# Kernel tuning notes

Hardware: AMD Instinct MI355X
Metric: run time of the kernel (lower is better)

The kernel has to match this reference:

```python
import jax, jax.numpy as jnp
import numpy as np

N, C, R = 100000, 128, 3
NUM_EMB = 3  # ceil((r+1)/2)+1 for r=3
E0, EL = 300000, 80000
SC = 0.05


def setup_inputs() -> dict:
    key = jax.random.key(0)
    ks = jax.random.split(key, 40)
    d = {}
    d["x"] = jax.random.normal(ks[0], (N, C), jnp.float32)
    # loopyN0: row 0 = sorted target node ids (CSR requirement), row 1 = neighbor ids
    t0 = jnp.sort(jax.random.randint(ks[1], (E0,), 0, N))
    s0 = jax.random.randint(ks[2], (E0,), 0, N)
    d["loopyN0"] = jnp.stack([t0, s0]).astype(jnp.int32)
    for L in range(1, R + 1):
        tgt = jnp.sort(jax.random.randint(ks[2 + 2 * L], (EL,), 0, N))
        rest = jax.random.randint(ks[3 + 2 * L], (L + 1, EL), 0, N)
        d[f"loopyN{L}"] = jnp.concatenate([tgt[None], rest]).astype(jnp.int32)
        d[f"loopyA{L}"] = jax.random.randint(ks[10 + L], (L + 2, EL), 0, NUM_EMB).astype(jnp.int32)
    # per-conv params (r=3 unshared CustomGINConv layers), stacked on leading axis
    d["emb"] = jax.random.normal(ks[20], (R, NUM_EMB, C)) * SC
    d["Wt"] = jax.random.normal(ks[21], (R, 2 * C, C)) * SC
    d["bt"] = jax.random.normal(ks[22], (R, C)) * SC
    d["mlp_w0"] = jax.random.normal(ks[23], (R, C, C)) * SC
    d["mlp_b0"] = jax.random.normal(ks[24], (R, C)) * SC
    d["mlp_w1"] = jax.random.normal(ks[25], (R, C, C)) * SC
    d["mlp_b1"] = jax.random.normal(ks[26], (R, C)) * SC
    d["conv_eps"] = jnp.ones((R,), jnp.float32)   # CustomGINConv eps init = ones(1)
    d["r_eps"] = jnp.zeros((R + 1,), jnp.float32)
    d["eps"] = jnp.zeros((), jnp.float32)
    # conv_final: MLP(C, C, num_layers=2, norm=Identity, relu)
    d["fin_w0"] = jax.random.normal(ks[27], (C, C)) * SC
    d["fin_b0"] = jax.random.normal(ks[28], (C,)) * SC
    d["fin_w1"] = jax.random.normal(ks[29], (C, C)) * SC
    d["fin_b1"] = jax.random.normal(ks[30], (C,)) * SC
    return d


def _mlp2(h, w0, b0, w1, b1):
    # MLP with num_layers=2, norm=Identity, relu
    h = h @ w0 + b0
    h = jax.nn.relu(h)
    return h @ w1 + b1


def reference(x, loopyN0, loopyN1, loopyN2, loopyN3, loopyA1, loopyA2, loopyA3,
              emb, Wt, bt, mlp_w0, mlp_b0, mlp_w1, mlp_b1,
              conv_eps, r_eps, eps, fin_w0, fin_b0, fin_w1, fin_b1):
    loopyN = [loopyN0, loopyN1, loopyN2, loopyN3]
    loopyA = [None, loopyA1, loopyA2, loopyA3]
    n_nodes = x.shape[0]
    # L = 0: plain neighbor sum (segment_csr over sorted targets == segment_sum)
    seg = jax.ops.segment_sum(x[loopyN0[1]], loopyN0[0], num_segments=n_nodes)
    rc = (1.0 + r_eps[0]) * seg
    for L in range(1, R + 1):
        nl = loopyN[L]
        cc = x[nl[1:]]                                  # [L+1, E, C] path-node gather
        at = loopyA[L][1:]                              # [L+1, E] atomic types
        i = L - 1
        h = jnp.concatenate([cc, emb[i][at]], axis=-1) @ Wt[i] + bt[i]   # [L+1, E, C]
        # custom_propagate: kernel [1,0,1] along path axis, zero 'same' padding
        hp = jnp.pad(h, ((1, 1), (0, 0), (0, 0)))
        y = hp[:-2] + hp[2:]
        o = _mlp2((1.0 + conv_eps[i]) * cc + y, mlp_w0[i], mlp_b0[i], mlp_w1[i], mlp_b1[i])
        o = o.sum(0)                                    # sum over path positions -> [E, C]
        seg = jax.ops.segment_sum(o, nl[0], num_segments=n_nodes)
        rc = rc + (1.0 + r_eps[L]) * seg
    return _mlp2((1.0 + eps) * x + rc, fin_w0, fin_b0, fin_w1, fin_b1)
```

## Files before the change

### kernel.cpp

```cpp
#include <hip/hip_runtime.h>
#include <stdint.h>

#define CDIM 128
#define NNODES 100000
#define E0EDGES 300000
#define ELEDGES 80000

typedef unsigned short u16;
typedef unsigned int u32;
typedef short bf16x8 __attribute__((ext_vector_type(8)));
typedef float f32x4 __attribute__((ext_vector_type(4)));

__device__ __forceinline__ float bf2f(u32 u){
  union { u32 i; float f; } v; v.i = u << 16; return v.f;
}
__device__ __forceinline__ float bf2f_hi(u32 u){
  union { u32 i; float f; } v; v.i = u & 0xffff0000u; return v.f;
}
__device__ __forceinline__ u16 f2bf(float f){
  u32 u = __builtin_bit_cast(u32, f);
  u32 r = (u + 0x7fffu + ((u >> 16) & 1u)) >> 16;
  return (u16)r;
}
__device__ __forceinline__ u32 pack2(float lo, float hi){
  return ((u32)f2bf(hi) << 16) | (u32)f2bf(lo);
}
__device__ __forceinline__ u32 cvtpk(float lo, float hi){
  u32 r;
  asm("v_cvt_pk_bf16_f32 %0, %1, %2" : "=v"(r) : "v"(lo), "v"(hi));
  return r;
}
template<int CTRL>
__device__ __forceinline__ float dppf(float v){
  int r = __builtin_amdgcn_update_dpp(0, __builtin_bit_cast(int, v), CTRL, 0xF, 0xF, true);
  return __builtin_bit_cast(float, r);
}
#define DPP_SHR1 0x111
#define DPP_SHL1 0x101
#define DPP_XOR1 0xB1
#define DPP_XOR2 0x4E

__device__ __forceinline__ int swzi(int r, int c){
  return r*CDIM + ((((c>>3) ^ (r&7)))<<3) + (c&7);
}
__device__ __forceinline__ int swz8(int r, int col0){
  int chunk = col0 >> 3;
  return r*CDIM + ((chunk ^ (r & 7)) << 3) + (col0 & 7);
}

__device__ __forceinline__ void gemm64(const u16* A, const u16* B, f32x4* acc, int wave, int lane){
  const int lr = lane & 15, g = lane >> 4;
  const int arow = wave*16 + lr;
#pragma unroll
  for (int ks = 0; ks < 4; ++ks){
    const int ach = ks*4 + g;
    bf16x8 a = *(const bf16x8*)&A[arow*CDIM + ((ach ^ (arow & 7)) << 3)];
#pragma unroll
    for (int ct = 0; ct < 8; ++ct){
      const int brow = ct*16 + lr;
      bf16x8 b = *(const bf16x8*)&B[brow*CDIM + ((ach ^ (brow & 7)) << 3)];
      acc[ct] = __builtin_amdgcn_mfma_f32_16x16x32_bf16(a, b, acc[ct], 0, 0, 0);
    }
  }
}

__device__ __forceinline__ void gemmS(const u16* W, const u16* Z, f32x4* acc, int zrow, int lane){
  const int lr = lane & 15, g = lane >> 4;
#pragma unroll
  for (int ks = 0; ks < 4; ++ks){
    const int ch = ks*4 + g;
    bf16x8 zb = *(const bf16x8*)&Z[zrow*CDIM + ((ch ^ (zrow & 7)) << 3)];
#pragma unroll
    for (int ct = 0; ct < 8; ++ct){
      const int wrow = ct*16 + lr;
      bf16x8 wb = *(const bf16x8*)&W[wrow*CDIM + ((ch ^ (wrow & 7)) << 3)];
      acc[ct] = __builtin_amdgcn_mfma_f32_16x16x32_bf16(wb, zb, acc[ct], 0, 0, 0);
    }
  }
}

__device__ __forceinline__ void stage_w(const u16* __restrict__ gsrc, u16* sdst, int tid){
  for (int c = tid; c < CDIM*16; c += 256){
    int r = c >> 4, ch = c & 15;
    *(uint4*)&sdst[(r*16 + (ch ^ (r & 7)))*8] = ((const uint4*)(gsrc + r*CDIM))[ch];
  }
}

__global__ __launch_bounds__(256) void xb_kernel(const float* __restrict__ x, u16* __restrict__ xb){
  int i = blockIdx.x*256 + threadIdx.x;
  size_t idx = (size_t)i*4;
  if (idx < (size_t)NNODES*CDIM){
    float4 v = *(const float4*)(x + idx);
    uint2 o; o.x = cvtpk(v.x, v.y); o.y = cvtpk(v.z, v.w);
    *(uint2*)(xb + idx) = o;
  }
}

__global__ __launch_bounds__(256) void prep_kernel(
    const float* __restrict__ Wt, const float* __restrict__ w0, const float* __restrict__ w1,
    const float* __restrict__ fw0, const float* __restrict__ fw1,
    const float* __restrict__ emb, const float* __restrict__ bt,
    u16* __restrict__ WtT, u16* __restrict__ w0T, u16* __restrict__ w1T,
    u16* __restrict__ fw0T, u16* __restrict__ fw1T, float* __restrict__ eWt)
{
  int tid = blockIdx.x*blockDim.x + threadIdx.x;
  int nt = gridDim.x*blockDim.x;
  for (int idx = tid; idx < 3*CDIM*CDIM; idx += nt){
    int i = idx/(CDIM*CDIM), rem = idx%(CDIM*CDIM), col = rem/CDIM, k = rem%CDIM;
    WtT[idx] = f2bf(Wt[(size_t)i*2*CDIM*CDIM + k*CDIM + col]);
    w0T[idx] = f2bf(w0[(size_t)i*CDIM*CDIM + k*CDIM + col]);
    w1T[idx] = f2bf(w1[(size_t)i*CDIM*CDIM + k*CDIM + col]);
  }
  for (int idx = tid; idx < CDIM*CDIM; idx += nt){
    int col = idx/CDIM, k = idx%CDIM;
    fw0T[idx] = f2bf(fw0[k*CDIM + col]);
    fw1T[idx] = f2bf(fw1[k*CDIM + col]);
  }
  for (int idx = tid; idx < 3*3*CDIM; idx += nt){
    int i = idx/(3*CDIM), a = (idx/CDIM)%3, c2 = idx%CDIM;
    float s = bt[i*CDIM + c2];
    for (int k = 0; k < CDIM; ++k)
      s += emb[(i*3 + a)*CDIM + k] * Wt[(size_t)i*2*CDIM*CDIM + (CDIM + k)*CDIM + c2];
    eWt[idx] = s;
  }
}

__global__ __launch_bounds__(256) void build_csr_kernel(
    const int* __restrict__ tgt, int ne, int* __restrict__ rowptr)
{
  int e = blockIdx.x*blockDim.x + threadIdx.x;
  if (e >= ne) return;
  int tc = tgt[e];
  int tp = (e == 0) ? -1 : tgt[e-1];
  for (int n = tp + 1; n <= tc; ++n) rowptr[n] = e;
  if (e == ne - 1){
    for (int n = tc + 1; n <= NNODES; ++n) rowptr[n] = ne;
  }
}

template<int L>
__global__ __launch_bounds__(512, 4) void layer_kernel(
    const u16* __restrict__ xb,
    const int* __restrict__ nl,
    const int* __restrict__ ai,
    const u16* __restrict__ WtT, const u16* __restrict__ w0T, const u16* __restrict__ w1T,
    const float* __restrict__ eWt,
    const float* __restrict__ b0g, const float* __restrict__ b1g,
    const float* __restrict__ cepsg,
    u16* __restrict__ oL)
{
  constexpr int RPE = (L == 1) ? 2 : 4;
  constexpr int TE  = 128 / RPE;
  constexpr int LI  = L - 1;
  __shared__ __align__(16) u16 sW[CDIM*CDIM];
  __shared__ __align__(16) u16 sA[128*CDIM];
  __shared__ __align__(16) float sE[3*136];
  __shared__ __align__(16) float b0s[CDIM];
  __shared__ __align__(16) float b1s[CDIM];

  const int tid  = threadIdx.x;
  const int wave = tid >> 6, lane = tid & 63;
  const int lr   = lane & 15, g = lane >> 4;
  const int row  = wave*16 + lr;
  const int e0   = blockIdx.x * TE;
  const int ed   = e0 + row / RPE;
  const int pos  = row % RPE;

  int node = -1, aid = 0;
  if (pos <= L){
    node = nl[(1 + pos)*ELEDGES + ed];
    aid  = ai[(1 + pos)*ELEDGES + ed];
  }
  const float mu = (pos > 0) ? 1.f : 0.f;
  const float md = (pos < L) ? 1.f : 0.f;
  const float ce = 1.0f + cepsg[LI];

  for (int c = tid; c < CDIM*16; c += 512){
    int r = c >> 4, ch = c & 15;
    *(uint4*)&sW[(r*16 + (ch ^ (r & 7)))*8] = ((const uint4*)(WtT + LI*CDIM*CDIM + r*CDIM))[ch];
  }
  for (int c = tid; c < 3*CDIM; c += 512) sE[(c>>7)*136 + (c&127)] = eWt[LI*3*CDIM + c];
  if (tid < CDIM) b0s[tid] = b0g[LI*CDIM + tid];
  else if (tid < 2*CDIM) b1s[tid-CDIM] = b1g[LI*CDIM + (tid-CDIM)];

  {
    const uint4* src = (const uint4*)(xb + (size_t)(node < 0 ? 0 : node)*CDIM);
#pragma unroll
    for (int i2 = 0; i2 < 4; ++i2){
      int ch = g*4 + i2;
      uint4 v = make_uint4(0u,0u,0u,0u);
      if (node >= 0) v = src[ch];
      *(uint4*)&sA[(row*16 + (ch ^ (row & 7)))*8] = v;
    }
  }
  __syncthreads();

  f32x4 acc[8];
#pragma unroll
  for (int ct = 0; ct < 8; ++ct) acc[ct] = (f32x4){0.f,0.f,0.f,0.f};
  gemmS(sW, sA, acc, row, lane);

  {
    const float* eWrow = &sE[aid*136];
#pragma unroll
    for (int ct = 0; ct < 8; ++ct){
      const int col0 = ct*16 + g*4;
      float4 ew = *(const float4*)&eWrow[col0];
      float h0 = acc[ct][0] + ew.x;
      float h1 = acc[ct][1] + ew.y;
      float h2 = acc[ct][2] + ew.z;
      float h3 = acc[ct][3] + ew.w;
      float u0 = dppf<DPP_SHR1>(h0), u1 = dppf<DPP_SHR1>(h1),
            u2 = dppf<DPP_SHR1>(h2), u3 = dppf<DPP_SHR1>(h3);
      float d0 = dppf<DPP_SHL1>(h0), d1 = dppf<DPP_SHL1>(h1),
            d2 = dppf<DPP_SHL1>(h2), d3 = dppf<DPP_SHL1>(h3);
      uint2 ccv = *(const uint2*)&sA[swz8(row, col0)];
      float c0 = bf2f(ccv.x & 0xffffu), c1 = bf2f_hi(ccv.x);
      float c2 = bf2f(ccv.y & 0xffffu), c3 = bf2f_hi(ccv.y);
      float z0 = ce*c0 + mu*u0 + md*d0;
      float z1 = ce*c1 + mu*u1 + md*d1;
      float z2 = ce*c2 + mu*u2 + md*d2;
      float z3 = ce*c3 + mu*u3 + md*d3;
      uint2 zv; zv.x = cvtpk(z0, z1); zv.y = cvtpk(z2, z3);
      *(uint2*)&sA[swz8(row, col0)] = zv;
    }
  }
  __syncthreads();
  for (int c = tid; c < CDIM*16; c += 512){
    int r = c >> 4, ch = c & 15;
    *(uint4*)&sW[(r*16 + (ch ^ (r & 7)))*8] = ((const uint4*)(w0T + LI*CDIM*CDIM + r*CDIM))[ch];
  }
  __syncthreads();

#pragma unroll
  for (int ct = 0; ct < 8; ++ct) acc[ct] = (f32x4){0.f,0.f,0.f,0.f};
  gemmS(sW, sA, acc, row, lane);

#pragma unroll
  for (int ct = 0; ct < 8; ++ct){
    const int col0 = ct*16 + g*4;
    float4 bb = *(const float4*)&b0s[col0];
    float t0 = acc[ct][0] + bb.x; t0 = t0 > 0.f ? t0 : 0.f;
    float t1 = acc[ct][1] + bb.y; t1 = t1 > 0.f ? t1 : 0.f;
    float t2 = acc[ct][2] + bb.z; t2 = t2 > 0.f ? t2 : 0.f;
    float t3 = acc[ct][3] + bb.w; t3 = t3 > 0.f ? t3 : 0.f;
    uint2 tv; tv.x = cvtpk(t0, t1); tv.y = cvtpk(t2, t3);
    *(uint2*)&sA[swz8(row, col0)] = tv;
  }
  __syncthreads();
  for (int c = tid; c < CDIM*16; c += 512){
    int r = c >> 4, ch = c & 15;
    *(uint4*)&sW[(r*16 + (ch ^ (r & 7)))*8] = ((const uint4*)(w1T + LI*CDIM*CDIM + r*CDIM))[ch];
  }
  __syncthreads();

#pragma unroll
  for (int ct = 0; ct < 8; ++ct) acc[ct] = (f32x4){0.f,0.f,0.f,0.f};
  gemmS(sW, sA, acc, row, lane);

  const float mz = (L == 2 && pos == 3) ? 0.f : 1.f;
#pragma unroll
  for (int ct = 0; ct < 8; ++ct){
    const int col0 = ct*16 + g*4;
    float v0 = mz*acc[ct][0], v1 = mz*acc[ct][1], v2 = mz*acc[ct][2], v3 = mz*acc[ct][3];
    v0 += dppf<DPP_XOR1>(v0); v1 += dppf<DPP_XOR1>(v1);
    v2 += dppf<DPP_XOR1>(v2); v3 += dppf<DPP_XOR1>(v3);
    if constexpr (RPE == 4){
      v0 += dppf<DPP_XOR2>(v0); v1 += dppf<DPP_XOR2>(v1);
      v2 += dppf<DPP_XOR2>(v2); v3 += dppf<DPP_XOR2>(v3);
    }
    if (pos == 0){
      float4 bb = *(const float4*)&b1s[col0];
      const float nb = (float)(L + 1);
      uint2 ov;
      ov.x = cvtpk(v0 + nb*bb.x, v1 + nb*bb.y);
      ov.y = cvtpk(v2 + nb*bb.z, v3 + nb*bb.w);
      *(uint2*)(oL + (size_t)ed*CDIM + col0) = ov;
    }
  }
}

__global__ __launch_bounds__(256) void gather_rc_kernel(
    const float* __restrict__ x,
    const int* __restrict__ s0,
    const int* __restrict__ rp0, const int* __restrict__ rp1,
    const int* __restrict__ rp2, const int* __restrict__ rp3,
    const u16* __restrict__ o1, const u16* __restrict__ o2, const u16* __restrict__ o3,
    const float* __restrict__ repsg, u16* __restrict__ rcb)
{
  const int wave = threadIdx.x >> 6, lane = threadIdx.x & 63;
  const int node = blockIdx.x*4 + wave;
  if (node >= NNODES) return;
  float a0 = 0.f, a1 = 0.f;
  {
    const float sc = 1.f + repsg[0];
    int lo = rp0[node], hi = rp0[node+1];
    for (int e = lo; e < hi; ++e){
      int s = s0[e];
      float2 v = *(const float2*)(x + (size_t)s*CDIM + lane*2);
      a0 += sc*v.x; a1 += sc*v.y;
    }
  }
  const u16* os[3]  = {o1, o2, o3};
  const int* rps[3] = {rp1, rp2, rp3};
#pragma unroll
  for (int li = 0; li < 3; ++li){
    const float sc = 1.f + repsg[1+li];
    int lo = rps[li][node], hi = rps[li][node+1];
    for (int e = lo; e < hi; ++e){
      u32 v = *(const u32*)(os[li] + (size_t)e*CDIM + lane*2);
      a0 += sc*bf2f(v & 0xffffu); a1 += sc*bf2f(v >> 16);
    }
  }
  *(u32*)(rcb + (size_t)node*CDIM + lane*2) = pack2(a0, a1);
}

__global__ __launch_bounds__(256) void final_kernel(
    const float* __restrict__ x, const u16* __restrict__ rc,
    const u16* __restrict__ fw0T, const u16* __restrict__ fw1T,
    const float* __restrict__ fb0, const float* __restrict__ fb1,
    const float* __restrict__ epsg, float* __restrict__ outp)
{
  __shared__ __align__(16) u16 sW[CDIM*CDIM];
  __shared__ __align__(16) u16 sA[64*CDIM];
  const int tid  = threadIdx.x;
  const int wave = tid >> 6, lane = tid & 63;
  const int lr   = lane & 15, g = lane >> 4;
  const int r0   = blockIdx.x * 64;
  const float se = 1.0f + epsg[0];

  stage_w(fw0T, sW, tid);
  for (int c = tid; c < 64*16; c += 256){
    int r = c >> 4, ch = c & 15;
    int node = r0 + r;
    uint4 v = make_uint4(0,0,0,0);
    if (node < NNODES){
      const float4* px = (const float4*)(x + (size_t)node*CDIM + ch*8);
      float4 fa = px[0], fb = px[1];
      const u32* pr = (const u32*)(rc + (size_t)node*CDIM + ch*8);
      u32 r0v = pr[0], r1v = pr[1], r2v = pr[2], r3v = pr[3];
      v.x = pack2(se*fa.x + bf2f(r0v & 0xffffu), se*fa.y + bf2f(r0v >> 16));
      v.y = pack2(se*fa.z + bf2f(r1v & 0xffffu), se*fa.w + bf2f(r1v >> 16));
      v.z = pack2(se*fb.x + bf2f(r2v & 0xffffu), se*fb.y + bf2f(r2v >> 16));
      v.w = pack2(se*fb.z + bf2f(r3v & 0xffffu), se*fb.w + bf2f(r3v >> 16));
    }
    *(uint4*)&sA[(r*16 + (ch ^ (r & 7)))*8] = v;
  }
  __syncthreads();

  f32x4 acc[8];
#pragma unroll
  for (int ct = 0; ct < 8; ++ct) acc[ct] = (f32x4){0.f,0.f,0.f,0.f};
  gemm64(sA, sW, acc, wave, lane);
  __syncthreads();
#pragma unroll
  for (int ct = 0; ct < 8; ++ct){
    const int col = ct*16 + lr;
    const float bb = fb0[col];
#pragma unroll
    for (int q = 0; q < 4; ++q){
      const int r = wave*16 + g*4 + q;
      float t = acc[ct][q] + bb;
      t = t > 0.f ? t : 0.f;
      sA[swzi(r, col)] = f2bf(t);
    }
  }
  stage_w(fw1T, sW, tid);
  __syncthreads();
#pragma unroll
  for (int ct = 0; ct < 8; ++ct) acc[ct] = (f32x4){0.f,0.f,0.f,0.f};
  gemm64(sA, sW, acc, wave, lane);
#pragma unroll
  for (int ct = 0; ct < 8; ++ct){
    const int col = ct*16 + lr;
    const float bb = fb1[col];
#pragma unroll
    for (int q = 0; q < 4; ++q){
      const int r = wave*16 + g*4 + q;
      int node = r0 + r;
      if (node < NNODES) outp[(size_t)node*CDIM + col] = acc[ct][q] + bb;
    }
  }
}

extern "C" void kernel_launch(void* const* d_in, const int* in_sizes, int n_in,
                              void* d_out, int out_size, void* d_ws, size_t ws_size,
                              hipStream_t stream)
{
  const float* x   = (const float*)d_in[0];
  const int* n0    = (const int*)d_in[1];
  const int* n1    = (const int*)d_in[2];
  const int* a1    = (const int*)d_in[3];
  const int* n2    = (const int*)d_in[4];
  const int* a2    = (const int*)d_in[5];
  const int* n3    = (const int*)d_in[6];
  const int* a3    = (const int*)d_in[7];
  const float* emb = (const float*)d_in[8];
  const float* Wt  = (const float*)d_in[9];
  const float* bt  = (const float*)d_in[10];
  const float* w0  = (const float*)d_in[11];
  const float* b0  = (const float*)d_in[12];
  const float* w1  = (const float*)d_in[13];
  const float* b1  = (const float*)d_in[14];
  const float* ceps= (const float*)d_in[15];
  const float* reps= (const float*)d_in[16];
  const float* eps = (const float*)d_in[17];
  const float* fw0 = (const float*)d_in[18];
  const float* fb0 = (const float*)d_in[19];
  const float* fw1 = (const float*)d_in[20];
  const float* fb1 = (const float*)d_in[21];
  float* outp = (float*)d_out;

  char* w = (char*)d_ws;
  size_t off = 0;
  auto alloc = [&](size_t bytes) -> char* {
    char* p = w + off;
    off += (bytes + 255) & ~((size_t)255);
    return p;
  };
  u16* o1   = (u16*)alloc((size_t)ELEDGES*CDIM*2);
  u16* o2   = (u16*)alloc((size_t)ELEDGES*CDIM*2);
  u16* o3   = (u16*)alloc((size_t)ELEDGES*CDIM*2);
  u16* rcb  = (u16*)alloc((size_t)NNODES*CDIM*2);
  int* rp0  = (int*)alloc((size_t)(NNODES+1)*4);
  int* rp1  = (int*)alloc((size_t)(NNODES+1)*4);
  int* rp2  = (int*)alloc((size_t)(NNODES+1)*4);
  int* rp3  = (int*)alloc((size_t)(NNODES+1)*4);
  u16* WtT  = (u16*)alloc((size_t)3*CDIM*CDIM*2);
  u16* w0T  = (u16*)alloc((size_t)3*CDIM*CDIM*2);
  u16* w1T  = (u16*)alloc((size_t)3*CDIM*CDIM*2);
  u16* fw0T = (u16*)alloc((size_t)CDIM*CDIM*2);
  u16* fw1T = (u16*)alloc((size_t)CDIM*CDIM*2);
  float* eWt = (float*)alloc((size_t)3*3*CDIM*4);
  u16* xb   = rcb;
  (void)ws_size; (void)in_sizes; (void)n_in; (void)out_size;

  prep_kernel<<<192, 256, 0, stream>>>(Wt, w0, w1, fw0, fw1, emb, bt,
                                       WtT, w0T, w1T, fw0T, fw1T, eWt);
  xb_kernel<<<(NNODES*CDIM/4 + 255)/256, 256, 0, stream>>>(x, xb);
  build_csr_kernel<<<(E0EDGES+255)/256, 256, 0, stream>>>(n0, E0EDGES, rp0);
  build_csr_kernel<<<(ELEDGES+255)/256, 256, 0, stream>>>(n1, ELEDGES, rp1);
  build_csr_kernel<<<(ELEDGES+255)/256, 256, 0, stream>>>(n2, ELEDGES, rp2);
  build_csr_kernel<<<(ELEDGES+255)/256, 256, 0, stream>>>(n3, ELEDGES, rp3);

  layer_kernel<1><<<ELEDGES/64, 512, 0, stream>>>(xb, n1, a1, WtT, w0T, w1T, eWt, b0, b1, ceps, o1);
  layer_kernel<2><<<ELEDGES/32, 512, 0, stream>>>(xb, n2, a2, WtT, w0T, w1T, eWt, b0, b1, ceps, o2);
  layer_kernel<3><<<ELEDGES/32, 512, 0, stream>>>(xb, n3, a3, WtT, w0T, w1T, eWt, b0, b1, ceps, o3);

  gather_rc_kernel<<<(NNODES+3)/4, 256, 0, stream>>>(x, n0 + E0EDGES, rp0, rp1, rp2, rp3,
                                                     o1, o2, o3, reps, rcb);
  final_kernel<<<(NNODES+63)/64, 256, 0, stream>>>(x, rcb, fw0T, fw1T, fb0, fb1, eps, outp);
}
```

Measured before the change: 436.6 us.

## Retile layer GEMMs to 2x2 wave grid, prefetch weights, fuse aux kernels

```diff
diff --git a/kernel.cpp b/kernel.cpp
--- a/kernel.cpp
+++ b/kernel.cpp
@@ -48,6 +48,31 @@
   return r*CDIM + ((chunk ^ (r & 7)) << 3) + (col0 & 7);
 }
 
+__device__ __forceinline__ void gemm4(const u16* W, const u16* A, f32x4 acc[4][4],
+                                      int rowbase, int featbase, int lr, int g){
+#pragma unroll
+  for (int ks = 0; ks < 4; ++ks){
+    const int ch = ks*4 + g;
+    const int sch = (ch ^ (lr & 7)) << 3;
+    bf16x8 af[4], wf[4];
+#pragma unroll
+    for (int a = 0; a < 4; ++a){
+      const int r = rowbase + 16*a + lr;
+      af[a] = *(const bf16x8*)&A[r*CDIM + sch];
+    }
+#pragma unroll
+    for (int b = 0; b < 4; ++b){
+      const int wr = featbase + 16*b + lr;
+      wf[b] = *(const bf16x8*)&W[wr*CDIM + sch];
+    }
+#pragma unroll
+    for (int a = 0; a < 4; ++a)
+#pragma unroll
+      for (int b = 0; b < 4; ++b)
+        acc[a][b] = __builtin_amdgcn_mfma_f32_16x16x32_bf16(wf[b], af[a], acc[a][b], 0, 0, 0);
+  }
+}
+
 __device__ __forceinline__ void gemm64(const u16* A, const u16* B, f32x4* acc, int wave, int lane){
   const int lr = lane & 15, g = lane >> 4;
   const int arow = wave*16 + lr;
@@ -64,35 +89,10 @@
   }
 }
 
-__device__ __forceinline__ void gemmS(const u16* W, const u16* Z, f32x4* acc, int zrow, int lane){
-  const int lr = lane & 15, g = lane >> 4;
-#pragma unroll
-  for (int ks = 0; ks < 4; ++ks){
-    const int ch = ks*4 + g;
-    bf16x8 zb = *(const bf16x8*)&Z[zrow*CDIM + ((ch ^ (zrow & 7)) << 3)];
-#pragma unroll
-    for (int ct = 0; ct < 8; ++ct){
-      const int wrow = ct*16 + lr;
-      bf16x8 wb = *(const bf16x8*)&W[wrow*CDIM + ((ch ^ (wrow & 7)) << 3)];
-      acc[ct] = __builtin_amdgcn_mfma_f32_16x16x32_bf16(wb, zb, acc[ct], 0, 0, 0);
-    }
-  }
-}
-
 __device__ __forceinline__ void stage_w(const u16* __restrict__ gsrc, u16* sdst, int tid){
   for (int c = tid; c < CDIM*16; c += 256){
     int r = c >> 4, ch = c & 15;
     *(uint4*)&sdst[(r*16 + (ch ^ (r & 7)))*8] = ((const uint4*)(gsrc + r*CDIM))[ch];
-  }
-}
-
-__global__ __launch_bounds__(256) void xb_kernel(const float* __restrict__ x, u16* __restrict__ xb){
-  int i = blockIdx.x*256 + threadIdx.x;
-  size_t idx = (size_t)i*4;
-  if (idx < (size_t)NNODES*CDIM){
-    float4 v = *(const float4*)(x + idx);
-    uint2 o; o.x = cvtpk(v.x, v.y); o.y = cvtpk(v.z, v.w);
-    *(uint2*)(xb + idx) = o;
   }
 }
 
@@ -125,11 +125,39 @@
   }
 }
 
-__global__ __launch_bounds__(256) void build_csr_kernel(
-    const int* __restrict__ tgt, int ne, int* __restrict__ rowptr)
+__global__ __launch_bounds__(256) void aux_kernel(
+    const float* __restrict__ x, u16* __restrict__ xb,
+    const int* __restrict__ n0, const int* __restrict__ n1,
+    const int* __restrict__ n2, const int* __restrict__ n3,
+    int* __restrict__ rp0, int* __restrict__ rp1,
+    int* __restrict__ rp2, int* __restrict__ rp3)
 {
-  int e = blockIdx.x*blockDim.x + threadIdx.x;
-  if (e >= ne) return;
+  const int XBQ = NNODES*CDIM/4;
+  int gtid = blockIdx.x*256 + threadIdx.x;
+  if (gtid < XBQ){
+    size_t idx = (size_t)gtid*4;
+    float4 v = *(const float4*)(x + idx);
+    uint2 o; o.x = cvtpk(v.x, v.y); o.y = cvtpk(v.z, v.w);
+    *(uint2*)(xb + idx) = o;
+    return;
+  }
+  int t = gtid - XBQ;
+  const int* tgt; int ne; int* rowptr;
+  if (t < E0EDGES){ tgt = n0; ne = E0EDGES; rowptr = rp0; }
+  else {
+    t -= E0EDGES;
+    if (t < ELEDGES){ tgt = n1; ne = ELEDGES; rowptr = rp1; }
+    else {
+      t -= ELEDGES;
+      if (t < ELEDGES){ tgt = n2; ne = ELEDGES; rowptr = rp2; }
+      else {
+        t -= ELEDGES;
+        if (t < ELEDGES){ tgt = n3; ne = ELEDGES; rowptr = rp3; }
+        else return;
+      }
+    }
+  }
+  int e = t;
   int tc = tgt[e];
   int tp = (e == 0) ? -1 : tgt[e-1];
   for (int n = tp + 1; n <= tc; ++n) rowptr[n] = e;
@@ -139,7 +167,7 @@
 }
 
 template<int L>
-__global__ __launch_bounds__(512, 4) void layer_kernel(
+__global__ __launch_bounds__(256, 2) void layer_kernel(
     const u16* __restrict__ xb,
     const int* __restrict__ nl,
     const int* __restrict__ ai,
@@ -157,131 +185,158 @@
   __shared__ __align__(16) float sE[3*136];
   __shared__ __align__(16) float b0s[CDIM];
   __shared__ __align__(16) float b1s[CDIM];
+  __shared__ int sAid[128];
 
   const int tid  = threadIdx.x;
   const int wave = tid >> 6, lane = tid & 63;
   const int lr   = lane & 15, g = lane >> 4;
-  const int row  = wave*16 + lr;
+  const int wr   = wave >> 1, wc = wave & 1;
+  const int rowbase  = wr*64;
+  const int featbase = wc*64;
   const int e0   = blockIdx.x * TE;
-  const int ed   = e0 + row / RPE;
-  const int pos  = row % RPE;
-
-  int node = -1, aid = 0;
-  if (pos <= L){
-    node = nl[(1 + pos)*ELEDGES + ed];
-    aid  = ai[(1 + pos)*ELEDGES + ed];
-  }
+  const int pos  = lr & (RPE - 1);
   const float mu = (pos > 0) ? 1.f : 0.f;
   const float md = (pos < L) ? 1.f : 0.f;
+  const float mz = (L == 2 && pos == 3) ? 0.f : 1.f;
   const float ce = 1.0f + cepsg[LI];
 
-  for (int c = tid; c < CDIM*16; c += 512){
-    int r = c >> 4, ch = c & 15;
-    *(uint4*)&sW[(r*16 + (ch ^ (r & 7)))*8] = ((const uint4*)(WtT + LI*CDIM*CDIM + r*CDIM))[ch];
-  }
-  for (int c = tid; c < 3*CDIM; c += 512) sE[(c>>7)*136 + (c&127)] = eWt[LI*3*CDIM + c];
+  stage_w(WtT + LI*CDIM*CDIM, sW, tid);
+  for (int c = tid; c < 3*CDIM; c += 256) sE[(c>>7)*136 + (c&127)] = eWt[LI*3*CDIM + c];
   if (tid < CDIM) b0s[tid] = b0g[LI*CDIM + tid];
   else if (tid < 2*CDIM) b1s[tid-CDIM] = b1g[LI*CDIM + (tid-CDIM)];
-
-  {
-    const uint4* src = (const uint4*)(xb + (size_t)(node < 0 ? 0 : node)*CDIM);
-#pragma unroll
-    for (int i2 = 0; i2 < 4; ++i2){
-      int ch = g*4 + i2;
-      uint4 v = make_uint4(0u,0u,0u,0u);
-      if (node >= 0) v = src[ch];
-      *(uint4*)&sA[(row*16 + (ch ^ (row & 7)))*8] = v;
-    }
-  }
-  __syncthreads();
-
-  f32x4 acc[8];
-#pragma unroll
-  for (int ct = 0; ct < 8; ++ct) acc[ct] = (f32x4){0.f,0.f,0.f,0.f};
-  gemmS(sW, sA, acc, row, lane);
-
-  {
-    const float* eWrow = &sE[aid*136];
-#pragma unroll
-    for (int ct = 0; ct < 8; ++ct){
-      const int col0 = ct*16 + g*4;
+  if (tid < 128){
+    int p = tid & (RPE - 1);
+    sAid[tid] = (p <= L) ? ai[(1 + p)*ELEDGES + e0 + tid/RPE] : 0;
+  }
+  for (int c = tid; c < 128*16; c += 256){
+    int r = c >> 4, ch = c & 15;
+    int p = r & (RPE - 1);
+    uint4 v = make_uint4(0u,0u,0u,0u);
+    if (p <= L){
+      int node = nl[(1 + p)*ELEDGES + e0 + r/RPE];
+      v = ((const uint4*)(xb + (size_t)node*CDIM))[ch];
+    }
+    *(uint4*)&sA[(r*16 + (ch ^ (r & 7)))*8] = v;
+  }
+  uint4 wpre[8];
+#pragma unroll
+  for (int i = 0; i < 8; ++i){
+    int c = tid + i*256;
+    wpre[i] = ((const uint4*)(w0T + LI*CDIM*CDIM + (c>>4)*CDIM))[c & 15];
+  }
+  __syncthreads();
+
+  f32x4 acc[4][4];
+#pragma unroll
+  for (int a = 0; a < 4; ++a)
+#pragma unroll
+    for (int b = 0; b < 4; ++b) acc[a][b] = (f32x4){0.f,0.f,0.f,0.f};
+  gemm4(sW, sA, acc, rowbase, featbase, lr, g);
+  __syncthreads();
+
+#pragma unroll
+  for (int i = 0; i < 8; ++i){
+    int c = tid + i*256;
+    int r = c >> 4, ch = c & 15;
+    *(uint4*)&sW[(r*16 + (ch ^ (r & 7)))*8] = wpre[i];
+  }
+#pragma unroll
+  for (int a = 0; a < 4; ++a){
+    const int r = rowbase + 16*a + lr;
+    const float* eWrow = &sE[sAid[r]*136];
+#pragma unroll
+    for (int b = 0; b < 4; ++b){
+      const int col0 = featbase + 16*b + g*4;
       float4 ew = *(const float4*)&eWrow[col0];
-      float h0 = acc[ct][0] + ew.x;
-      float h1 = acc[ct][1] + ew.y;
-      float h2 = acc[ct][2] + ew.z;
-      float h3 = acc[ct][3] + ew.w;
+      float h0 = acc[a][b][0] + ew.x;
+      float h1 = acc[a][b][1] + ew.y;
+      float h2 = acc[a][b][2] + ew.z;
+      float h3 = acc[a][b][3] + ew.w;
       float u0 = dppf<DPP_SHR1>(h0), u1 = dppf<DPP_SHR1>(h1),
             u2 = dppf<DPP_SHR1>(h2), u3 = dppf<DPP_SHR1>(h3);
       float d0 = dppf<DPP_SHL1>(h0), d1 = dppf<DPP_SHL1>(h1),
             d2 = dppf<DPP_SHL1>(h2), d3 = dppf<DPP_SHL1>(h3);
-      uint2 ccv = *(const uint2*)&sA[swz8(row, col0)];
+      uint2 ccv = *(const uint2*)&sA[swz8(r, col0)];
       float c0 = bf2f(ccv.x & 0xffffu), c1 = bf2f_hi(ccv.x);
       float c2 = bf2f(ccv.y & 0xffffu), c3 = bf2f_hi(ccv.y);
-      float z0 = ce*c0 + mu*u0 + md*d0;
-      float z1 = ce*c1 + mu*u1 + md*d1;
-      float z2 = ce*c2 + mu*u2 + md*d2;
-      float z3 = ce*c3 + mu*u3 + md*d3;
-      uint2 zv; zv.x = cvtpk(z0, z1); zv.y = cvtpk(z2, z3);
-      *(uint2*)&sA[swz8(row, col0)] = zv;
-    }
-  }
-  __syncthreads();
-  for (int c = tid; c < CDIM*16; c += 512){
+      uint2 zv;
+      zv.x = cvtpk(ce*c0 + mu*u0 + md*d0, ce*c1 + mu*u1 + md*d1);
+      zv.y = cvtpk(ce*c2 + mu*u2 + md*d2, ce*c3 + mu*u3 + md*d3);
+      *(uint2*)&sA[swz8(r, col0)] = zv;
+    }
+  }
+  __syncthreads();
+
+#pragma unroll
+  for (int a = 0; a < 4; ++a)
+#pragma unroll
+    for (int b = 0; b < 4; ++b) acc[a][b] = (f32x4){0.f,0.f,0.f,0.f};
+#pragma unroll
+  for (int i = 0; i < 8; ++i){
+    int c = tid + i*256;
+    wpre[i] = ((const uint4*)(w1T + LI*CDIM*CDIM + (c>>4)*CDIM))[c & 15];
+  }
+  gemm4(sW, sA, acc, rowbase, featbase, lr, g);
+  __syncthreads();
+
+#pragma unroll
+  for (int i = 0; i < 8; ++i){
+    int c = tid + i*256;
     int r = c >> 4, ch = c & 15;
-    *(uint4*)&sW[(r*16 + (ch ^ (r & 7)))*8] = ((const uint4*)(w0T + LI*CDIM*CDIM + r*CDIM))[ch];
-  }
-  __syncthreads();
-
-#pragma unroll
-  for (int ct = 0; ct < 8; ++ct) acc[ct] = (f32x4){0.f,0.f,0.f,0.f};
-  gemmS(sW, sA, acc, row, lane);
-
-#pragma unroll
-  for (int ct = 0; ct < 8; ++ct){
-    const int col0 = ct*16 + g*4;
-    float4 bb = *(const float4*)&b0s[col0];
-    float t0 = acc[ct][0] + bb.x; t0 = t0 > 0.f ? t0 : 0.f;
-    float t1 = acc[ct][1] + bb.y; t1 = t1 > 0.f ? t1 : 0.f;
-    float t2 = acc[ct][2] + bb.z; t2 = t2 > 0.f ? t2 : 0.f;
-    float t3 = acc[ct][3] + bb.w; t3 = t3 > 0.f ? t3 : 0.f;
-    uint2 tv; tv.x = cvtpk(t0, t1); tv.y = cvtpk(t2, t3);
-    *(uint2*)&sA[swz8(row, col0)] = tv;
-  }
-  __syncthreads();
-  for (int c = tid; c < CDIM*16; c += 512){
-    int r = c >> 4, ch = c & 15;
-    *(uint4*)&sW[(r*16 + (ch ^ (r & 7)))*8] = ((const uint4*)(w1T + LI*CDIM*CDIM + r*CDIM))[ch];
-  }
-  __syncthreads();
-
-#pragma unroll
-  for (int ct = 0; ct < 8; ++ct) acc[ct] = (f32x4){0.f,0.f,0.f,0.f};
-  gemmS(sW, sA, acc, row, lane);
-
-  const float mz = (L == 2 && pos == 3) ? 0.f : 1.f;
-#pragma unroll
-  for (int ct = 0; ct < 8; ++ct){
-    const int col0 = ct*16 + g*4;
-    float v0 = mz*acc[ct][0], v1 = mz*acc[ct][1], v2 = mz*acc[ct][2], v3 = mz*acc[ct][3];
-    v0 += dppf<DPP_XOR1>(v0); v1 += dppf<DPP_XOR1>(v1);
-    v2 += dppf<DPP_XOR1>(v2); v3 += dppf<DPP_XOR1>(v3);
-    if constexpr (RPE == 4){
-      v0 += dppf<DPP_XOR2>(v0); v1 += dppf<DPP_XOR2>(v1);
-      v2 += dppf<DPP_XOR2>(v2); v3 += dppf<DPP_XOR2>(v3);
-    }
-    if (pos == 0){
-      float4 bb = *(const float4*)&b1s[col0];
-      const float nb = (float)(L + 1);
-      uint2 ov;
-      ov.x = cvtpk(v0 + nb*bb.x, v1 + nb*bb.y);
-      ov.y = cvtpk(v2 + nb*bb.z, v3 + nb*bb.w);
-      *(uint2*)(oL + (size_t)ed*CDIM + col0) = ov;
+    *(uint4*)&sW[(r*16 + (ch ^ (r & 7)))*8] = wpre[i];
+  }
+#pragma unroll
+  for (int a = 0; a < 4; ++a){
+    const int r = rowbase + 16*a + lr;
+#pragma unroll
+    for (int b = 0; b < 4; ++b){
+      const int col0 = featbase + 16*b + g*4;
+      float4 bb = *(const float4*)&b0s[col0];
+      float t0 = acc[a][b][0] + bb.x; t0 = t0 > 0.f ? t0 : 0.f;
+      float t1 = acc[a][b][1] + bb.y; t1 = t1 > 0.f ? t1 : 0.f;
+      float t2 = acc[a][b][2] + bb.z; t2 = t2 > 0.f ? t2 : 0.f;
+      float t3 = acc[a][b][3] + bb.w; t3 = t3 > 0.f ? t3 : 0.f;
+      uint2 tv; tv.x = cvtpk(t0, t1); tv.y = cvtpk(t2, t3);
+      *(uint2*)&sA[swz8(r, col0)] = tv;
+    }
+  }
+  __syncthreads();
+
+#pragma unroll
+  for (int a = 0; a < 4; ++a)
+#pragma unroll
+    for (int b = 0; b < 4; ++b) acc[a][b] = (f32x4){0.f,0.f,0.f,0.f};
+  gemm4(sW, sA, acc, rowbase, featbase, lr, g);
+
+  const float nb = (float)(L + 1);
+#pragma unroll
+  for (int a = 0; a < 4; ++a){
+    const int r = rowbase + 16*a + lr;
+    const int ed = e0 + r/RPE;
+#pragma unroll
+    for (int b = 0; b < 4; ++b){
+      float v0 = mz*acc[a][b][0], v1 = mz*acc[a][b][1],
+            v2 = mz*acc[a][b][2], v3 = mz*acc[a][b][3];
+      v0 += dppf<DPP_XOR1>(v0); v1 += dppf<DPP_XOR1>(v1);
+      v2 += dppf<DPP_XOR1>(v2); v3 += dppf<DPP_XOR1>(v3);
+      if constexpr (RPE == 4){
+        v0 += dppf<DPP_XOR2>(v0); v1 += dppf<DPP_XOR2>(v1);
+        v2 += dppf<DPP_XOR2>(v2); v3 += dppf<DPP_XOR2>(v3);
+      }
+      if (pos == 0){
+        const int col0 = featbase + 16*b + g*4;
+        float4 bb = *(const float4*)&b1s[col0];
+        uint2 ov;
+        ov.x = cvtpk(v0 + nb*bb.x, v1 + nb*bb.y);
+        ov.y = cvtpk(v2 + nb*bb.z, v3 + nb*bb.w);
+        *(uint2*)(oL + (size_t)ed*CDIM + col0) = ov;
+      }
     }
   }
 }
 
 __global__ __launch_bounds__(256) void gather_rc_kernel(
-    const float* __restrict__ x,
+    const float* __restrict__ x, const u16* __restrict__ xbopt,
     const int* __restrict__ s0,
     const int* __restrict__ rp0, const int* __restrict__ rp1,
     const int* __restrict__ rp2, const int* __restrict__ rp3,
@@ -295,10 +350,18 @@
   {
     const float sc = 1.f + repsg[0];
     int lo = rp0[node], hi = rp0[node+1];
-    for (int e = lo; e < hi; ++e){
-      int s = s0[e];
-      float2 v = *(const float2*)(x + (size_t)s*CDIM + lane*2);
-      a0 += sc*v.x; a1 += sc*v.y;
+    if (xbopt){
+      for (int e = lo; e < hi; ++e){
+        int s = s0[e];
+        u32 v = *(const u32*)(xbopt + (size_t)s*CDIM + lane*2);
+        a0 += sc*bf2f(v & 0xffffu); a1 += sc*bf2f_hi(v);
+      }
+    } else {
+      for (int e = lo; e < hi; ++e){
+        int s = s0[e];
+        float2 v = *(const float2*)(x + (size_t)s*CDIM + lane*2);
+        a0 += sc*v.x; a1 += sc*v.y;
+      }
     }
   }
   const u16* os[3]  = {o1, o2, o3};
@@ -309,7 +372,7 @@
     int lo = rps[li][node], hi = rps[li][node+1];
     for (int e = lo; e < hi; ++e){
       u32 v = *(const u32*)(os[li] + (size_t)e*CDIM + lane*2);
-      a0 += sc*bf2f(v & 0xffffu); a1 += sc*bf2f(v >> 16);
+      a0 += sc*bf2f(v & 0xffffu); a1 += sc*bf2f_hi(v);
     }
   }
   *(u32*)(rcb + (size_t)node*CDIM + lane*2) = pack2(a0, a1);
@@ -339,10 +402,10 @@
       float4 fa = px[0], fb = px[1];
       const u32* pr = (const u32*)(rc + (size_t)node*CDIM + ch*8);
       u32 r0v = pr[0], r1v = pr[1], r2v = pr[2], r3v = pr[3];
-      v.x = pack2(se*fa.x + bf2f(r0v & 0xffffu), se*fa.y + bf2f(r0v >> 16));
-      v.y = pack2(se*fa.z + bf2f(r1v & 0xffffu), se*fa.w + bf2f(r1v >> 16));
-      v.z = pack2(se*fb.x + bf2f(r2v & 0xffffu), se*fb.y + bf2f(r2v >> 16));
-      v.w = pack2(se*fb.z + bf2f(r3v & 0xffffu), se*fb.w + bf2f(r3v >> 16));
+      v.x = pack2(se*fa.x + bf2f(r0v & 0xffffu), se*fa.y + bf2f_hi(r0v));
+      v.y = pack2(se*fa.z + bf2f(r1v & 0xffffu), se*fa.w + bf2f_hi(r1v));
+      v.z = pack2(se*fb.x + bf2f(r2v & 0xffffu), se*fb.y + bf2f_hi(r2v));
+      v.w = pack2(se*fb.z + bf2f(r3v & 0xffffu), se*fb.w + bf2f_hi(r3v));
     }
     *(uint4*)&sA[(r*16 + (ch ^ (r & 7)))*8] = v;
   }
@@ -432,22 +495,26 @@
   u16* fw0T = (u16*)alloc((size_t)CDIM*CDIM*2);
   u16* fw1T = (u16*)alloc((size_t)CDIM*CDIM*2);
   float* eWt = (float*)alloc((size_t)3*3*CDIM*4);
-  u16* xb   = rcb;
-  (void)ws_size; (void)in_sizes; (void)n_in; (void)out_size;
+  const size_t xbbytes = (size_t)NNODES*CDIM*2;
+  u16* xb; const u16* xbopt;
+  if (off + xbbytes <= ws_size){ xb = (u16*)alloc(xbbytes); xbopt = xb; }
+  else { xb = rcb; xbopt = nullptr; }
+  (void)in_sizes; (void)n_in; (void)out_size;
 
   prep_kernel<<<192, 256, 0, stream>>>(Wt, w0, w1, fw0, fw1, emb, bt,
                                        WtT, w0T, w1T, fw0T, fw1T, eWt);
-  xb_kernel<<<(NNODES*CDIM/4 + 255)/256, 256, 0, stream>>>(x, xb);
-  build_csr_kernel<<<(E0EDGES+255)/256, 256, 0, stream>>>(n0, E0EDGES, rp0);
-  build_csr_kernel<<<(ELEDGES+255)/256, 256, 0, stream>>>(n1, ELEDGES, rp1);
-  build_csr_kernel<<<(ELEDGES+255)/256, 256, 0, stream>>>(n2, ELEDGES, rp2);
-  build_csr_kernel<<<(ELEDGES+255)/256, 256, 0, stream>>>(n3, ELEDGES, rp3);
-
-  layer_kernel<1><<<ELEDGES/64, 512, 0, stream>>>(xb, n1, a1, WtT, w0T, w1T, eWt, b0, b1, ceps, o1);
-  layer_kernel<2><<<ELEDGES/32, 512, 0, stream>>>(xb, n2, a2, WtT, w0T, w1T, eWt, b0, b1, ceps, o2);
-  layer_kernel<3><<<ELEDGES/32, 512, 0, stream>>>(xb, n3, a3, WtT, w0T, w1T, eWt, b0, b1, ceps, o3);
-
-  gather_rc_kernel<<<(NNODES+3)/4, 256, 0, stream>>>(x, n0 + E0EDGES, rp0, rp1, rp2, rp3,
+  {
+    const int XBQ = NNODES*CDIM/4;
+    int total = XBQ + E0EDGES + 3*ELEDGES;
+    aux_kernel<<<(total + 255)/256, 256, 0, stream>>>(x, xb, n0, n1, n2, n3,
+                                                      rp0, rp1, rp2, rp3);
+  }
+
+  layer_kernel<1><<<ELEDGES/64, 256, 0, stream>>>(xb, n1, a1, WtT, w0T, w1T, eWt, b0, b1, ceps, o1);
+  layer_kernel<2><<<ELEDGES/32, 256, 0, stream>>>(xb, n2, a2, WtT, w0T, w1T, eWt, b0, b1, ceps, o2);
+  layer_kernel<3><<<ELEDGES/32, 256, 0, stream>>>(xb, n3, a3, WtT, w0T, w1T, eWt, b0, b1, ceps, o3);
+
+  gather_rc_kernel<<<(NNODES+3)/4, 256, 0, stream>>>(x, xbopt, n0 + E0EDGES, rp0, rp1, rp2, rp3,
                                                      o1, o2, o3, reps, rcb);
   final_kernel<<<(NNODES+63)/64, 256, 0, stream>>>(x, rcb, fw0T, fw1T, fb0, fb1, eps, outp);
 }
```

Result: slower. 517.4 us (+18.5%).
